# Kernel tuning notes

Hardware: AMD Instinct MI355X
Metric: run time of the kernel (lower is better)

## Reference

```python
import jax, jax.numpy as jnp
import numpy as np

NHID, NHEAD, HEAD_DIM, U = 512, 16, 64, 3  # U = unfold_size (hardcoded 3 in original)
B, L = 8, 2048
D = NHEAD * HEAD_DIM  # 1024


def setup_inputs() -> dict:
    key = jax.random.key(0)
    ks = jax.random.split(key, 9)
    s = 0.02
    return {
        "x": jax.random.normal(ks[0], (B, NHID, L, 1), jnp.float32),
        "wq": jax.random.normal(ks[1], (NHID, D), jnp.float32) * s,
        "bq": jnp.zeros((D,), jnp.float32),
        "wk": jax.random.normal(ks[2], (NHID, D), jnp.float32) * s,
        "bk": jnp.zeros((D,), jnp.float32),
        "wv": jax.random.normal(ks[3], (NHID, D), jnp.float32) * s,
        "bv": jnp.zeros((D,), jnp.float32),
        "wo": jax.random.normal(ks[4], (D, NHID), jnp.float32) * s,
        "bo": jnp.zeros((NHID,), jnp.float32),
    }


def _unfold(t):
    # t: (B, D, L). Replicates tf.image.extract_patches (ksize 3, SAME, zero pad)
    # followed by the original's reshape (B,L,1,D,3) -- which reinterprets the
    # window-major flat layout (w*D + c) as (c', w') -- then transpose to
    # (B, D, 3, L) and reshape to (B, nhead, head_dim, 3, L).
    b, d, l = t.shape
    tt = jnp.transpose(t, (0, 2, 1))                  # (B, L, D)
    tp = jnp.pad(tt, ((0, 0), (1, 1), (0, 0)))        # SAME zero padding along L
    p = jnp.stack([tp[:, w:w + l, :] for w in range(U)], axis=2)  # (B, L, 3, D), flat idx = w*D + c
    p = p.reshape(b, l, d, U)                         # faithful reinterpreting reshape
    p = jnp.transpose(p, (0, 2, 3, 1))                # (B, D, 3, L)
    return p.reshape(b, NHEAD, HEAD_DIM, U, l)


def reference(x, wq, bq, wk, bk, wv, bv, wo, bo):
    b, c, l, _ = x.shape
    xs = x[..., 0]                                    # (B, C, L)
    # 1x1 convs (channels_first) == channel matmuls
    q = jnp.einsum('bcl,cd->bdl', xs, wq) + bq[None, :, None]
    k = jnp.einsum('bcl,cd->bdl', xs, wk) + bk[None, :, None]
    v = jnp.einsum('bcl,cd->bdl', xs, wv) + bv[None, :, None]
    q = q.reshape(b, NHEAD, HEAD_DIM, 1, l)           # (B, nh, hd, 1, L)
    k = _unfold(k)                                    # (B, nh, hd, 3, L)
    v = _unfold(v)
    scale = jnp.sqrt(jnp.asarray(HEAD_DIM, x.dtype))
    alphas = jnp.sum(q * k, axis=2, keepdims=True) / scale  # (B, nh, 1, 3, L)
    alphas = jax.nn.softmax(alphas, axis=3)
    att = jnp.sum(alphas * v, axis=3)                 # (B, nh, hd, L)
    # faithful to original: transpose then reinterpreting reshape to (B, D, L)
    att = jnp.transpose(att, (0, 1, 3, 2)).reshape(b, D, l)
    ret = jnp.einsum('bdl,dc->bcl', att, wo) + bo[None, :, None]
    return ret[..., None]                             # (B, nhid, L, 1)
```

## Files before the change

### kernel.cpp

```cpp
#include <hip/hip_runtime.h>

typedef _Float16 f16_t;
typedef _Float16 f16x2 __attribute__((ext_vector_type(2)));
typedef _Float16 f16x8 __attribute__((ext_vector_type(8)));
typedef float floatx4 __attribute__((ext_vector_type(4)));
typedef unsigned int u32;
typedef const __attribute__((address_space(1))) unsigned int* gptr_as1;
typedef __attribute__((address_space(3))) unsigned int* lptr_as3;

#define B_ 8
#define C_ 512
#define L_ 2048
#define D_ 1024
#define H_ 16

static __device__ __forceinline__ f16x2 bc2(u32 v) { return __builtin_bit_cast(f16x2, v); }
static __device__ __forceinline__ u32 cb2(f16x2 v) { return __builtin_bit_cast(u32, v); }

__global__ __launch_bounds__(256) void _MSA1_ktransf2h(const float* __restrict__ in,
                                                       f16_t* __restrict__ out,
                                                       int R, int C) {
  size_t zoff = (size_t)blockIdx.z * R * C;
  in += zoff; out += zoff;
  __shared__ f16_t tile[64][65];
  int r0 = blockIdx.y * 64, c0 = blockIdx.x * 64;
  int t = threadIdx.x;
  #pragma unroll
  for (int i = 0; i < 16; ++i) {
    int idx = t + i * 256;
    int r = idx >> 6, c = idx & 63;
    tile[c][r] = (f16_t)in[(size_t)(r0 + r) * C + (c0 + c)];
  }
  __syncthreads();
  #pragma unroll
  for (int i = 0; i < 16; ++i) {
    int idx = t + i * 256;
    int r = idx >> 6, c = idx & 63;
    out[(size_t)(c0 + r) * R + (r0 + c)] = tile[r][c];
  }
}

__global__ __launch_bounds__(256) void _MSA1_ktransh(const f16_t* __restrict__ in,
                                                     f16_t* __restrict__ out,
                                                     int R, int C) {
  size_t zoff = (size_t)blockIdx.z * R * C;
  in += zoff; out += zoff;
  __shared__ f16_t tile[64][65];
  int r0 = blockIdx.y * 64, c0 = blockIdx.x * 64;
  int t = threadIdx.x;
  #pragma unroll
  for (int i = 0; i < 16; ++i) {
    int idx = t + i * 256;
    int r = idx >> 6, c = idx & 63;
    tile[c][r] = in[(size_t)(r0 + r) * C + (c0 + c)];
  }
  __syncthreads();
  #pragma unroll
  for (int i = 0; i < 16; ++i) {
    int idx = t + i * 256;
    int r = idx >> 6, c = idx & 63;
    out[(size_t)(c0 + r) * R + (r0 + c)] = tile[r][c];
  }
}

__global__ __launch_bounds__(256) void _MSA1_kbias3(const float* __restrict__ bq,
                                                    const float* __restrict__ bk,
                                                    const float* __restrict__ bv,
                                                    float* __restrict__ out) {
  for (int i = threadIdx.x; i < 1024; i += 256) {
    out[i] = bq[i];
    out[1024 + i] = bk[i];
    out[2048 + i] = bv[i];
  }
}

template <bool F32OUT, int K>
__global__ __launch_bounds__(256) void _MSA1_kgemm(
    const f16_t* __restrict__ A, const f16_t* __restrict__ Bt,
    const float* __restrict__ bias, void* __restrict__ Cdv,
    int M, int N, long sA, long sB, long sC) {
  A  += (size_t)blockIdx.z * sA;
  Bt += (size_t)blockIdx.z * sB;
  const int m0 = blockIdx.y * 128, n0 = blockIdx.x * 128;

  union ShU {
    struct { f16_t As[128][32]; f16_t Bs[128][32]; } ab;
    f16_t Ep[F32OUT ? 1 : 128][132];
  };
  __shared__ ShU sh;

  const int t = threadIdx.x;
  const int lane = t & 63, w = t >> 6;
  const int mh = (w & 1) * 64, nh = (w >> 1) * 64;
  const int fm = lane & 15, fq = lane >> 4;
  const int srcoff = ((t & 3) ^ ((t >> 2) & 3)) * 8;
  const int colf = ((fq ^ (fm & 3)) * 8);

  floatx4 acc[4][4];
  #pragma unroll
  for (int i = 0; i < 4; ++i)
    #pragma unroll
    for (int j = 0; j < 4; ++j) {
      floatx4 z4 = {0.f, 0.f, 0.f, 0.f};
      acc[i][j] = z4;
    }

  for (int kt = 0; kt < K; kt += 32) {
    __syncthreads();
    #pragma unroll
    for (int j = 0; j < 2; ++j) {
      int chunk = j * 256 + t;
      int r = chunk >> 2;
      const f16_t* ga = A + (size_t)(m0 + r) * K + kt + srcoff;
      __builtin_amdgcn_global_load_lds((gptr_as1)(const void*)ga,
          (lptr_as3)(void*)((char*)&sh.ab.As[0][0] + j * 4096 + w * 1024), 16, 0, 0);
      const f16_t* gb = Bt + (size_t)(n0 + r) * K + kt + srcoff;
      __builtin_amdgcn_global_load_lds((gptr_as1)(const void*)gb,
          (lptr_as3)(void*)((char*)&sh.ab.Bs[0][0] + j * 4096 + w * 1024), 16, 0, 0);
    }
    __syncthreads();

    f16x8 af[4], bfr[4];
    #pragma unroll
    for (int mt = 0; mt < 4; ++mt)
      af[mt] = *(const f16x8*)&sh.ab.As[mh + mt * 16 + fm][colf];
    #pragma unroll
    for (int nt = 0; nt < 4; ++nt)
      bfr[nt] = *(const f16x8*)&sh.ab.Bs[nh + nt * 16 + fm][colf];
    #pragma unroll
    for (int mt = 0; mt < 4; ++mt)
      #pragma unroll
      for (int nt = 0; nt < 4; ++nt)
        acc[mt][nt] = __builtin_amdgcn_mfma_f32_16x16x32_f16(
            af[mt], bfr[nt], acc[mt][nt], 0, 0, 0);
  }
  __syncthreads();

  if (F32OUT) {
    float* Cd = (float*)Cdv + (size_t)blockIdx.z * sC;
    #pragma unroll
    for (int mt = 0; mt < 4; ++mt) {
      float bv4[4];
      #pragma unroll
      for (int r = 0; r < 4; ++r)
        bv4[r] = bias[m0 + mh + mt * 16 + fq * 4 + r];
      #pragma unroll
      for (int nt = 0; nt < 4; ++nt) {
        int col = n0 + nh + nt * 16 + fm;
        #pragma unroll
        for (int r = 0; r < 4; ++r) {
          int row = m0 + mh + mt * 16 + fq * 4 + r;
          Cd[(size_t)row * N + col] = acc[mt][nt][r] + bv4[r];
        }
      }
    }
  } else {
    f16_t* Cd = (f16_t*)Cdv + (size_t)blockIdx.z * sC;
    #pragma unroll
    for (int mt = 0; mt < 4; ++mt) {
      float bv4[4];
      #pragma unroll
      for (int r = 0; r < 4; ++r)
        bv4[r] = bias[m0 + mh + mt * 16 + fq * 4 + r];
      #pragma unroll
      for (int nt = 0; nt < 4; ++nt) {
        int col = nh + nt * 16 + fm;
        #pragma unroll
        for (int r = 0; r < 4; ++r) {
          int row = mh + mt * 16 + fq * 4 + r;
          sh.Ep[row][col] = (f16_t)(acc[mt][nt][r] + bv4[r]);
        }
      }
    }
    __syncthreads();
    #pragma unroll
    for (int i = 0; i < 16; ++i) {
      int chunk = i * 256 + t;
      int row = chunk >> 5, c8 = chunk & 31;
      uint2 val = *(const uint2*)&sh.Ep[row][c8 * 4];
      *(uint2*)&Cd[(size_t)(m0 + row) * N + n0 + c8 * 4] = val;
    }
  }
}

template <bool EDGE>
__global__ __launch_bounds__(256) void _MSA1_kattn3(const f16_t* __restrict__ qkv,
                                                    f16_t* __restrict__ att,
                                                    int xmul, int xadd) {
  const int t = threadIdx.x;
  const int lane = t & 63;
  const int wid = __builtin_amdgcn_readfirstlane(t >> 6);
  const int h = blockIdx.y, b = blockIdx.z;
  const int lbase = (blockIdx.x * xmul + xadd) * 256;
  const int l0 = lbase + lane * 4;
  const size_t plane = (size_t)D_ * L_;
  const f16_t* base = qkv + (size_t)b * 3 * plane;

  __shared__ uint2 sred[4][3][64];
  __shared__ f16_t tile[256][66];

  const f16_t* qp = base + (size_t)(h * 64 + wid * 16) * L_ + l0;
  const f16_t* kpl = base + plane;
  const f16_t* vpl = base + 2 * plane;
  const int g0 = h * 192 + wid * 48;

  f16x2 sLo[3], sHi[3];
  #pragma unroll
  for (int w = 0; w < 3; ++w) { f16x2 z = {(f16_t)0, (f16_t)0}; sLo[w] = z; sHi[w] = z; }

  #pragma unroll
  for (int dd = 0; dd < 16; ++dd) {
    uint2 qw = *(const uint2*)(qp + (size_t)dd * L_);
    f16x2 qlo = bc2(qw.x), qhi = bc2(qw.y);
    #pragma unroll
    for (int w = 0; w < 3; ++w) {
      int g = g0 + 3 * dd + w;
      int c = g & 1023;
      int o = (g >> 10) - 1;
      uint2 kw = *(const uint2*)(kpl + (size_t)c * L_ + (l0 + o));
      if (EDGE) {
        if (o < 0 && l0 == 0) kw.x &= 0xFFFF0000u;
        if (o > 0 && l0 == 2044) kw.y &= 0x0000FFFFu;
      }
      sLo[w] = bc2(kw.x) * qlo + sLo[w];
      sHi[w] = bc2(kw.y) * qhi + sHi[w];
    }
  }
  #pragma unroll
  for (int w = 0; w < 3; ++w) {
    uint2 v; v.x = cb2(sLo[w]); v.y = cb2(sHi[w]);
    sred[wid][w][lane] = v;
  }
  __syncthreads();

  float sc[4][3];
  #pragma unroll
  for (int j = 0; j < 3; ++j) {
    uint2 r0 = sred[0][j][lane], r1 = sred[1][j][lane];
    uint2 r2 = sred[2][j][lane], r3 = sred[3][j][lane];
    f16x2 lo = (bc2(r0.x) + bc2(r1.x)) + (bc2(r2.x) + bc2(r3.x));
    f16x2 hi = (bc2(r0.y) + bc2(r1.y)) + (bc2(r2.y) + bc2(r3.y));
    sc[0][j] = (float)lo.x * 0.125f;
    sc[1][j] = (float)lo.y * 0.125f;
    sc[2][j] = (float)hi.x * 0.125f;
    sc[3][j] = (float)hi.y * 0.125f;
  }
  f16_t ef[4][3];
  #pragma unroll
  for (int li = 0; li < 4; ++li) {
    float mx = fmaxf(sc[li][0], fmaxf(sc[li][1], sc[li][2]));
    float e0 = __expf(sc[li][0] - mx), e1 = __expf(sc[li][1] - mx), e2 = __expf(sc[li][2] - mx);
    float inv = 1.f / (e0 + e1 + e2);
    ef[li][0] = (f16_t)(e0 * inv); ef[li][1] = (f16_t)(e1 * inv); ef[li][2] = (f16_t)(e2 * inv);
  }
  f16x2 eLo[3], eHi[3];
  #pragma unroll
  for (int w = 0; w < 3; ++w) {
    f16x2 a = {ef[0][w], ef[1][w]}; eLo[w] = a;
    f16x2 b2 = {ef[2][w], ef[3][w]}; eHi[w] = b2;
  }

  #pragma unroll
  for (int dd = 0; dd < 16; ++dd) {
    f16x2 aLo = {(f16_t)0, (f16_t)0}, aHi = {(f16_t)0, (f16_t)0};
    #pragma unroll
    for (int w = 0; w < 3; ++w) {
      int g = g0 + 3 * dd + w;
      int c = g & 1023;
      int o = (g >> 10) - 1;
      uint2 vw = *(const uint2*)(vpl + (size_t)c * L_ + (l0 + o));
      if (EDGE) {
        if (o < 0 && l0 == 0) vw.x &= 0xFFFF0000u;
        if (o > 0 && l0 == 2044) vw.y &= 0x0000FFFFu;
      }
      aLo = bc2(vw.x) * eLo[w] + aLo;
      aHi = bc2(vw.y) * eHi[w] + aHi;
    }
    int d = wid * 16 + dd;
    tile[lane * 4 + 0][d] = aLo.x;
    tile[lane * 4 + 1][d] = aLo.y;
    tile[lane * 4 + 2][d] = aHi.x;
    tile[lane * 4 + 3][d] = aHi.y;
  }
  __syncthreads();

  f16_t* ob = att + ((size_t)(b * H_ + h) * L_ + lbase) * 64;
  #pragma unroll
  for (int i = 0; i < 8; ++i) {
    int idx = i * 256 + t;
    int row = idx >> 3, seg = idx & 7;
    const u32* src = (const u32*)&tile[row][seg * 8];
    uint4 val;
    val.x = src[0]; val.y = src[1]; val.z = src[2]; val.w = src[3];
    *(uint4*)(ob + (size_t)row * 64 + seg * 8) = val;
  }
}

extern "C" void kernel_launch(void* const* d_in, const int* in_sizes, int n_in,
                              void* d_out, int out_size, void* d_ws, size_t ws_size,
                              hipStream_t stream) {
  (void)in_sizes; (void)n_in; (void)out_size;
  const float* x  = (const float*)d_in[0];
  const float* wq = (const float*)d_in[1];
  const float* bq = (const float*)d_in[2];
  const float* wk = (const float*)d_in[3];
  const float* bk = (const float*)d_in[4];
  const float* wv = (const float*)d_in[5];
  const float* bv = (const float*)d_in[6];
  const float* wo = (const float*)d_in[7];
  const float* bo = (const float*)d_in[8];
  float* out = (float*)d_out;
  char* ws = (char*)d_ws;

  f16_t* wT3   = (f16_t*)(ws);
  f16_t* woT   = (f16_t*)(ws + 3145728);
  float* bias3 = (float*) (ws + 4194304);
  const size_t SHARED_END = 4210688;

  _MSA1_kbias3<<<dim3(1), dim3(256), 0, stream>>>(bq, bk, bv, bias3);
  _MSA1_ktransf2h<<<dim3(16, 8, 1), dim3(256), 0, stream>>>(wq, wT3, 512, 1024);
  _MSA1_ktransf2h<<<dim3(16, 8, 1), dim3(256), 0, stream>>>(wk, wT3 + 524288, 512, 1024);
  _MSA1_ktransf2h<<<dim3(16, 8, 1), dim3(256), 0, stream>>>(wv, wT3 + 1048576, 512, 1024);
  _MSA1_ktransf2h<<<dim3(8, 16, 1), dim3(256), 0, stream>>>(wo, woT, 1024, 512);

  if (ws_size >= 188760064ull) {
    f16_t* xT    = (f16_t*)(ws + SHARED_END);
    f16_t* qkv   = xT + 8388608ull;
    f16_t* att2  = qkv + 50331648ull;
    f16_t* att2T = att2 + 16777216ull;

    _MSA1_ktransf2h<<<dim3(32, 8, B_), dim3(256), 0, stream>>>(x, xT, 512, 2048);
    _MSA1_kgemm<false, 512><<<dim3(16, 24, B_), dim3(256), 0, stream>>>(
        wT3, xT, bias3, qkv, 3072, 2048,
        0L, (long)(2048 * 512), (long)(3072 * 2048));
    _MSA1_kattn3<false><<<dim3(6, 16, B_), dim3(256), 0, stream>>>(qkv, att2, 1, 1);
    _MSA1_kattn3<true><<<dim3(2, 16, B_), dim3(256), 0, stream>>>(qkv, att2, 7, 0);
    _MSA1_ktransh<<<dim3(32, 16, B_), dim3(256), 0, stream>>>(att2, att2T, 1024, 2048);
    _MSA1_kgemm<true, 1024><<<dim3(16, 4, B_), dim3(256), 0, stream>>>(
        woT, att2T, bo, out, 512, 2048,
        0L, (long)(2048 * 1024), (long)(512 * 2048));
  } else {
    f16_t* xTb    = (f16_t*)(ws + SHARED_END);
    f16_t* qkvb   = xTb + 1048576ull;
    f16_t* att2b  = qkvb + 6291456ull;
    f16_t* att2Tb = att2b + 2097152ull;
    for (int b = 0; b < B_; ++b) {
      const float* xb = x + (size_t)b * C_ * L_;
      _MSA1_ktransf2h<<<dim3(32, 8, 1), dim3(256), 0, stream>>>(xb, xTb, 512, 2048);
      _MSA1_kgemm<false, 512><<<dim3(16, 24, 1), dim3(256), 0, stream>>>(
          wT3, xTb, bias3, qkvb, 3072, 2048, 0L, 0L, 0L);
      _MSA1_kattn3<false><<<dim3(6, 16, 1), dim3(256), 0, stream>>>(qkvb, att2b, 1, 1);
      _MSA1_kattn3<true><<<dim3(2, 16, 1), dim3(256), 0, stream>>>(qkvb, att2b, 7, 0);
      _MSA1_ktransh<<<dim3(32, 16, 1), dim3(256), 0, stream>>>(att2b, att2Tb, 1024, 2048);
      _MSA1_kgemm<true, 1024><<<dim3(16, 4, 1), dim3(256), 0, stream>>>(
          woT, att2Tb, bo, out + (size_t)b * C_ * L_, 512, 2048, 0L, 0L, 0L);
    }
  }
}
```

Baseline: 296.7 us.

## Fuse weight-prep launches and deepen GEMM K-tile to 64 with XOR swizzle

Merges the bias copy and four weight transpose/convert launches into one grid, removing four kernel launches. The GEMM K-step doubles from 32 to 64, with an 8-way XOR swizzle on the LDS layout and two MFMA sub-steps per tile, which halves the number of barrier pairs per output tile. The trade-off is doubled LDS use per block, which may lower occupancy.

```diff
diff --git a/kernel.cpp b/kernel.cpp
--- a/kernel.cpp
+++ b/kernel.cpp
@@ -63,14 +63,48 @@
   }
 }
 
-__global__ __launch_bounds__(256) void _MSA1_kbias3(const float* __restrict__ bq,
-                                                    const float* __restrict__ bk,
-                                                    const float* __restrict__ bv,
-                                                    float* __restrict__ out) {
-  for (int i = threadIdx.x; i < 1024; i += 256) {
-    out[i] = bq[i];
-    out[1024 + i] = bk[i];
-    out[2048 + i] = bv[i];
+__global__ __launch_bounds__(256) void _MSA1_kprep(
+    const float* __restrict__ wq, const float* __restrict__ wk,
+    const float* __restrict__ wv, const float* __restrict__ wo,
+    const float* __restrict__ bq, const float* __restrict__ bk,
+    const float* __restrict__ bv,
+    f16_t* __restrict__ wT3, f16_t* __restrict__ woT, float* __restrict__ bias3) {
+  const int x = blockIdx.x, y = blockIdx.y;
+  const int t = threadIdx.x;
+  if (x == 128) {
+    if (y == 0) {
+      for (int i = t; i < 1024; i += 256) {
+        bias3[i] = bq[i];
+        bias3[1024 + i] = bk[i];
+        bias3[2048 + i] = bv[i];
+      }
+    }
+    return;
+  }
+  __shared__ f16_t tile[64][65];
+  const float* in; f16_t* out; int R, C, r0, c0;
+  if (y < 3) {
+    R = 512; C = 1024;
+    in = (y == 0) ? wq : (y == 1) ? wk : wv;
+    out = wT3 + (size_t)y * 524288;
+    r0 = (x >> 4) * 64; c0 = (x & 15) * 64;
+  } else {
+    R = 1024; C = 512;
+    in = wo; out = woT;
+    r0 = (x >> 3) * 64; c0 = (x & 7) * 64;
+  }
+  #pragma unroll
+  for (int i = 0; i < 16; ++i) {
+    int idx = t + i * 256;
+    int r = idx >> 6, c = idx & 63;
+    tile[c][r] = (f16_t)in[(size_t)(r0 + r) * C + (c0 + c)];
+  }
+  __syncthreads();
+  #pragma unroll
+  for (int i = 0; i < 16; ++i) {
+    int idx = t + i * 256;
+    int r = idx >> 6, c = idx & 63;
+    out[(size_t)(c0 + r) * R + (r0 + c)] = tile[r][c];
   }
 }
 
@@ -84,7 +118,7 @@
   const int m0 = blockIdx.y * 128, n0 = blockIdx.x * 128;
 
   union ShU {
-    struct { f16_t As[128][32]; f16_t Bs[128][32]; } ab;
+    struct { f16_t As[128][64]; f16_t Bs[128][64]; } ab;
     f16_t Ep[F32OUT ? 1 : 128][132];
   };
   __shared__ ShU sh;
@@ -93,8 +127,6 @@
   const int lane = t & 63, w = t >> 6;
   const int mh = (w & 1) * 64, nh = (w >> 1) * 64;
   const int fm = lane & 15, fq = lane >> 4;
-  const int srcoff = ((t & 3) ^ ((t >> 2) & 3)) * 8;
-  const int colf = ((fq ^ (fm & 3)) * 8);
 
   floatx4 acc[4][4];
   #pragma unroll
@@ -105,34 +137,42 @@
       acc[i][j] = z4;
     }
 
-  for (int kt = 0; kt < K; kt += 32) {
+  for (int kt = 0; kt < K; kt += 64) {
     __syncthreads();
     #pragma unroll
-    for (int j = 0; j < 2; ++j) {
-      int chunk = j * 256 + t;
-      int r = chunk >> 2;
-      const f16_t* ga = A + (size_t)(m0 + r) * K + kt + srcoff;
+    for (int j = 0; j < 4; ++j) {
+      int c = j * 256 + t;
+      int r = c >> 3;
+      int k8 = (((c & 7) ^ (r & 7)) * 8);
+      const f16_t* ga = A + (size_t)(m0 + r) * K + kt + k8;
       __builtin_amdgcn_global_load_lds((gptr_as1)(const void*)ga,
           (lptr_as3)(void*)((char*)&sh.ab.As[0][0] + j * 4096 + w * 1024), 16, 0, 0);
-      const f16_t* gb = Bt + (size_t)(n0 + r) * K + kt + srcoff;
+      const f16_t* gb = Bt + (size_t)(n0 + r) * K + kt + k8;
       __builtin_amdgcn_global_load_lds((gptr_as1)(const void*)gb,
           (lptr_as3)(void*)((char*)&sh.ab.Bs[0][0] + j * 4096 + w * 1024), 16, 0, 0);
     }
     __syncthreads();
 
-    f16x8 af[4], bfr[4];
-    #pragma unroll
-    for (int mt = 0; mt < 4; ++mt)
-      af[mt] = *(const f16x8*)&sh.ab.As[mh + mt * 16 + fm][colf];
-    #pragma unroll
-    for (int nt = 0; nt < 4; ++nt)
-      bfr[nt] = *(const f16x8*)&sh.ab.Bs[nh + nt * 16 + fm][colf];
-    #pragma unroll
-    for (int mt = 0; mt < 4; ++mt)
-      #pragma unroll
-      for (int nt = 0; nt < 4; ++nt)
-        acc[mt][nt] = __builtin_amdgcn_mfma_f32_16x16x32_f16(
-            af[mt], bfr[nt], acc[mt][nt], 0, 0, 0);
+    #pragma unroll
+    for (int ks = 0; ks < 2; ++ks) {
+      f16x8 af[4], bfr[4];
+      #pragma unroll
+      for (int mt = 0; mt < 4; ++mt) {
+        int row = mh + mt * 16 + fm;
+        af[mt] = *(const f16x8*)&sh.ab.As[row][(((ks * 4 + fq) ^ (row & 7)) * 8)];
+      }
+      #pragma unroll
+      for (int nt = 0; nt < 4; ++nt) {
+        int row = nh + nt * 16 + fm;
+        bfr[nt] = *(const f16x8*)&sh.ab.Bs[row][(((ks * 4 + fq) ^ (row & 7)) * 8)];
+      }
+      #pragma unroll
+      for (int mt = 0; mt < 4; ++mt)
+        #pragma unroll
+        for (int nt = 0; nt < 4; ++nt)
+          acc[mt][nt] = __builtin_amdgcn_mfma_f32_16x16x32_f16(
+              af[mt], bfr[nt], acc[mt][nt], 0, 0, 0);
+    }
   }
   __syncthreads();
 
@@ -317,11 +357,8 @@
   float* bias3 = (float*) (ws + 4194304);
   const size_t SHARED_END = 4210688;
 
-  _MSA1_kbias3<<<dim3(1), dim3(256), 0, stream>>>(bq, bk, bv, bias3);
-  _MSA1_ktransf2h<<<dim3(16, 8, 1), dim3(256), 0, stream>>>(wq, wT3, 512, 1024);
-  _MSA1_ktransf2h<<<dim3(16, 8, 1), dim3(256), 0, stream>>>(wk, wT3 + 524288, 512, 1024);
-  _MSA1_ktransf2h<<<dim3(16, 8, 1), dim3(256), 0, stream>>>(wv, wT3 + 1048576, 512, 1024);
-  _MSA1_ktransf2h<<<dim3(8, 16, 1), dim3(256), 0, stream>>>(wo, woT, 1024, 512);
+  _MSA1_kprep<<<dim3(129, 4), dim3(256), 0, stream>>>(
+      wq, wk, wv, wo, bq, bk, bv, wT3, woT, bias3);
 
   if (ws_size >= 188760064ull) {
     f16_t* xT    = (f16_t*)(ws + SHARED_END);
```

New measurement: 283.2 us. -4.6%, faster.

## Fuse attention output transpose into attention kernel and merge weight-prep launches

Applied to the files above, without the earlier changes.

The attention kernel now writes its output directly in the transposed (L, D) layout the output projection GEMM expects. This removes the separate half-precision transpose kernel and its extra 32 MB round trip through global memory. The bias copy and four weight-transpose launches are merged into one prep kernel, cutting launch count. The new attention stores are 16-byte writes strided by D, so each write covers only a small part of a row. That may hurt coalescing compared with the old contiguous writes.

```diff
diff --git a/kernel.cpp b/kernel.cpp
--- a/kernel.cpp
+++ b/kernel.cpp
@@ -40,19 +40,41 @@
   }
 }
 
-__global__ __launch_bounds__(256) void _MSA1_ktransh(const f16_t* __restrict__ in,
-                                                     f16_t* __restrict__ out,
-                                                     int R, int C) {
-  size_t zoff = (size_t)blockIdx.z * R * C;
-  in += zoff; out += zoff;
+__global__ __launch_bounds__(256) void _MSA1_kprep(
+    const float* __restrict__ wq, const float* __restrict__ wk,
+    const float* __restrict__ wv, const float* __restrict__ wo,
+    const float* __restrict__ bq, const float* __restrict__ bk,
+    const float* __restrict__ bv,
+    f16_t* __restrict__ wT3, f16_t* __restrict__ woT, float* __restrict__ bias3) {
+  const int x = blockIdx.x, y = blockIdx.y;
+  const int t = threadIdx.x;
+  if (x == 128) {
+    if (y == 0) {
+      for (int i = t; i < 1024; i += 256) {
+        bias3[i] = bq[i];
+        bias3[1024 + i] = bk[i];
+        bias3[2048 + i] = bv[i];
+      }
+    }
+    return;
+  }
   __shared__ f16_t tile[64][65];
-  int r0 = blockIdx.y * 64, c0 = blockIdx.x * 64;
-  int t = threadIdx.x;
+  const float* in; f16_t* out; int R, C, r0, c0;
+  if (y < 3) {
+    R = 512; C = 1024;
+    in = (y == 0) ? wq : (y == 1) ? wk : wv;
+    out = wT3 + (size_t)y * 524288;
+    r0 = (x >> 4) * 64; c0 = (x & 15) * 64;
+  } else {
+    R = 1024; C = 512;
+    in = wo; out = woT;
+    r0 = (x >> 3) * 64; c0 = (x & 7) * 64;
+  }
   #pragma unroll
   for (int i = 0; i < 16; ++i) {
     int idx = t + i * 256;
     int r = idx >> 6, c = idx & 63;
-    tile[c][r] = in[(size_t)(r0 + r) * C + (c0 + c)];
+    tile[c][r] = (f16_t)in[(size_t)(r0 + r) * C + (c0 + c)];
   }
   __syncthreads();
   #pragma unroll
@@ -60,17 +82,6 @@
     int idx = t + i * 256;
     int r = idx >> 6, c = idx & 63;
     out[(size_t)(c0 + r) * R + (r0 + c)] = tile[r][c];
-  }
-}
-
-__global__ __launch_bounds__(256) void _MSA1_kbias3(const float* __restrict__ bq,
-                                                    const float* __restrict__ bk,
-                                                    const float* __restrict__ bv,
-                                                    float* __restrict__ out) {
-  for (int i = threadIdx.x; i < 1024; i += 256) {
-    out[i] = bq[i];
-    out[1024 + i] = bk[i];
-    out[2048 + i] = bv[i];
   }
 }
 
@@ -184,20 +195,21 @@
 }
 
 template <bool EDGE>
-__global__ __launch_bounds__(256) void _MSA1_kattn3(const f16_t* __restrict__ qkv,
-                                                    f16_t* __restrict__ att,
+__global__ __launch_bounds__(256) void _MSA1_kattn5(const f16_t* __restrict__ qkv,
+                                                    f16_t* __restrict__ attT,
                                                     int xmul, int xadd) {
   const int t = threadIdx.x;
   const int lane = t & 63;
   const int wid = __builtin_amdgcn_readfirstlane(t >> 6);
   const int h = blockIdx.y, b = blockIdx.z;
-  const int lbase = (blockIdx.x * xmul + xadd) * 256;
+  const int chi = blockIdx.x * xmul + xadd;
+  const int lbase = chi * 256;
   const int l0 = lbase + lane * 4;
   const size_t plane = (size_t)D_ * L_;
   const f16_t* base = qkv + (size_t)b * 3 * plane;
 
   __shared__ uint2 sred[4][3][64];
-  __shared__ f16_t tile[256][66];
+  __shared__ __align__(16) f16_t tile2[2048][8];
 
   const f16_t* qp = base + (size_t)(h * 64 + wid * 16) * L_ + l0;
   const f16_t* kpl = base + plane;
@@ -260,6 +272,8 @@
     f16x2 b2 = {ef[2][w], ef[3][w]}; eHi[w] = b2;
   }
 
+  const int llb = (lane & 7) * 256 + wid * 16;
+  const int jcol = lane >> 3;
   #pragma unroll
   for (int dd = 0; dd < 16; ++dd) {
     f16x2 aLo = {(f16_t)0, (f16_t)0}, aHi = {(f16_t)0, (f16_t)0};
@@ -276,23 +290,20 @@
       aLo = bc2(vw.x) * eLo[w] + aLo;
       aHi = bc2(vw.y) * eHi[w] + aHi;
     }
-    int d = wid * 16 + dd;
-    tile[lane * 4 + 0][d] = aLo.x;
-    tile[lane * 4 + 1][d] = aLo.y;
-    tile[lane * 4 + 2][d] = aHi.x;
-    tile[lane * 4 + 3][d] = aHi.y;
-  }
-  __syncthreads();
-
-  f16_t* ob = att + ((size_t)(b * H_ + h) * L_ + lbase) * 64;
+    const int llq = llb + dd;
+    tile2[llq +   0][jcol] = aLo.x;
+    tile2[llq +  64][jcol] = aLo.y;
+    tile2[llq + 128][jcol] = aHi.x;
+    tile2[llq + 192][jcol] = aHi.y;
+  }
+  __syncthreads();
+
+  f16_t* ob = attT + (size_t)b * L_ * D_ + h * 64 + chi * 8;
   #pragma unroll
   for (int i = 0; i < 8; ++i) {
-    int idx = i * 256 + t;
-    int row = idx >> 3, seg = idx & 7;
-    const u32* src = (const u32*)&tile[row][seg * 8];
-    uint4 val;
-    val.x = src[0]; val.y = src[1]; val.z = src[2]; val.w = src[3];
-    *(uint4*)(ob + (size_t)row * 64 + seg * 8) = val;
+    int ll = i * 256 + t;
+    uint4 val = *(const uint4*)&tile2[ll][0];
+    *(uint4*)(ob + (size_t)ll * D_) = val;
   }
 }
 
@@ -317,41 +328,34 @@
   float* bias3 = (float*) (ws + 4194304);
   const size_t SHARED_END = 4210688;
 
-  _MSA1_kbias3<<<dim3(1), dim3(256), 0, stream>>>(bq, bk, bv, bias3);
-  _MSA1_ktransf2h<<<dim3(16, 8, 1), dim3(256), 0, stream>>>(wq, wT3, 512, 1024);
-  _MSA1_ktransf2h<<<dim3(16, 8, 1), dim3(256), 0, stream>>>(wk, wT3 + 524288, 512, 1024);
-  _MSA1_ktransf2h<<<dim3(16, 8, 1), dim3(256), 0, stream>>>(wv, wT3 + 1048576, 512, 1024);
-  _MSA1_ktransf2h<<<dim3(8, 16, 1), dim3(256), 0, stream>>>(wo, woT, 1024, 512);
-
-  if (ws_size >= 188760064ull) {
+  _MSA1_kprep<<<dim3(129, 4), dim3(256), 0, stream>>>(
+      wq, wk, wv, wo, bq, bk, bv, wT3, woT, bias3);
+
+  if (ws_size >= 155205632ull) {
     f16_t* xT    = (f16_t*)(ws + SHARED_END);
     f16_t* qkv   = xT + 8388608ull;
-    f16_t* att2  = qkv + 50331648ull;
-    f16_t* att2T = att2 + 16777216ull;
+    f16_t* att2T = qkv + 50331648ull;
 
     _MSA1_ktransf2h<<<dim3(32, 8, B_), dim3(256), 0, stream>>>(x, xT, 512, 2048);
     _MSA1_kgemm<false, 512><<<dim3(16, 24, B_), dim3(256), 0, stream>>>(
         wT3, xT, bias3, qkv, 3072, 2048,
         0L, (long)(2048 * 512), (long)(3072 * 2048));
-    _MSA1_kattn3<false><<<dim3(6, 16, B_), dim3(256), 0, stream>>>(qkv, att2, 1, 1);
-    _MSA1_kattn3<true><<<dim3(2, 16, B_), dim3(256), 0, stream>>>(qkv, att2, 7, 0);
-    _MSA1_ktransh<<<dim3(32, 16, B_), dim3(256), 0, stream>>>(att2, att2T, 1024, 2048);
+    _MSA1_kattn5<false><<<dim3(6, 16, B_), dim3(256), 0, stream>>>(qkv, att2T, 1, 1);
+    _MSA1_kattn5<true><<<dim3(2, 16, B_), dim3(256), 0, stream>>>(qkv, att2T, 7, 0);
     _MSA1_kgemm<true, 1024><<<dim3(16, 4, B_), dim3(256), 0, stream>>>(
         woT, att2T, bo, out, 512, 2048,
         0L, (long)(2048 * 1024), (long)(512 * 2048));
   } else {
     f16_t* xTb    = (f16_t*)(ws + SHARED_END);
     f16_t* qkvb   = xTb + 1048576ull;
-    f16_t* att2b  = qkvb + 6291456ull;
-    f16_t* att2Tb = att2b + 2097152ull;
+    f16_t* att2Tb = qkvb + 6291456ull;
     for (int b = 0; b < B_; ++b) {
       const float* xb = x + (size_t)b * C_ * L_;
       _MSA1_ktransf2h<<<dim3(32, 8, 1), dim3(256), 0, stream>>>(xb, xTb, 512, 2048);
       _MSA1_kgemm<false, 512><<<dim3(16, 24, 1), dim3(256), 0, stream>>>(
           wT3, xTb, bias3, qkvb, 3072, 2048, 0L, 0L, 0L);
-      _MSA1_kattn3<false><<<dim3(6, 16, 1), dim3(256), 0, stream>>>(qkvb, att2b, 1, 1);
-      _MSA1_kattn3<true><<<dim3(2, 16, 1), dim3(256), 0, stream>>>(qkvb, att2b, 7, 0);
-      _MSA1_ktransh<<<dim3(32, 16, 1), dim3(256), 0, stream>>>(att2b, att2Tb, 1024, 2048);
+      _MSA1_kattn5<false><<<dim3(6, 16, 1), dim3(256), 0, stream>>>(qkvb, att2Tb, 1, 1);
+      _MSA1_kattn5<true><<<dim3(2, 16, 1), dim3(256), 0, stream>>>(qkvb, att2Tb, 7, 0);
       _MSA1_kgemm<true, 1024><<<dim3(16, 4, 1), dim3(256), 0, stream>>>(
           woT, att2Tb, bo, out + (size_t)b * C_ * L_, 512, 2048, 0L, 0L, 0L);
     }
```

Result: faster. 285.3 us (-3.8%).
